# Kernel tuning notes

Measured on AMD Instinct MI355X. Metric: run time of the kernel, lower is better.

## Reference

```python
import jax, jax.numpy as jnp
import numpy as np

B, S, E = 4, 2048, 1024
H, Dh = 16, 64


def setup_inputs() -> dict:
    key = jax.random.key(0)
    ks = jax.random.split(key, 9)
    scale_in = 1.0 / np.sqrt(E)
    scale_out = 1.0 / np.sqrt(H * Dh)
    x = jax.random.normal(ks[0], (B, S, E), dtype=jnp.float32)
    # Per-head projection weights stacked over heads: [H, E, Dh]
    Wq = jax.random.uniform(ks[1], (H, E, Dh), jnp.float32, -scale_in, scale_in)
    bq = jax.random.uniform(ks[2], (H, Dh), jnp.float32, -scale_in, scale_in)
    Wk = jax.random.uniform(ks[3], (H, E, Dh), jnp.float32, -scale_in, scale_in)
    bk = jax.random.uniform(ks[4], (H, Dh), jnp.float32, -scale_in, scale_in)
    Wv = jax.random.uniform(ks[5], (H, E, Dh), jnp.float32, -scale_in, scale_in)
    bv = jax.random.uniform(ks[6], (H, Dh), jnp.float32, -scale_in, scale_in)
    # Output projection: [H*Dh, E]
    Wo = jax.random.uniform(ks[7], (H * Dh, E), jnp.float32, -scale_out, scale_out)
    bo = jax.random.uniform(ks[8], (E,), jnp.float32, -scale_out, scale_out)
    return {"x": x, "Wq": Wq, "bq": bq, "Wk": Wk, "bk": bk,
            "Wv": Wv, "bv": bv, "Wo": Wo, "bo": bo}


def reference(x, Wq, bq, Wk, bk, Wv, bv, Wo, bo):
    # Per-head linear projections, batched over heads: [B, H, S, Dh]
    q = jnp.einsum('bse,hed->bhsd', x, Wq) + bq[None, :, None, :]
    k = jnp.einsum('bse,hed->bhsd', x, Wk) + bk[None, :, None, :]
    v = jnp.einsum('bse,hed->bhsd', x, Wv) + bv[None, :, None, :]
    scale = 1.0 / jnp.sqrt(jnp.asarray(Dh, dtype=x.dtype))
    scores = jnp.einsum('bhsd,bhtd->bhst', q, k) * scale  # [B, H, S, S]
    weights = jax.nn.softmax(scores, axis=-1)
    z = jnp.einsum('bhst,bhtd->bhsd', weights, v)  # [B, H, S, Dh]
    # Concat heads in module order: [B, S, H*Dh]
    z = jnp.transpose(z, (0, 2, 1, 3)).reshape(B, S, H * Dh)
    return z @ Wo + bo
```

## Files before the change

### kernel.cpp

```cpp
#include <hip/hip_runtime.h>
#include <hip/hip_bf16.h>

#define B_  4
#define S_  2048
#define E_  1024
#define H_  16
#define DH_ 64
#define M_  (B_*S_)
#define HD_ (H_*DH_)

typedef unsigned short u16;
typedef __attribute__((ext_vector_type(8))) __bf16 bf16x8;
typedef __attribute__((ext_vector_type(4))) __bf16 bf16x4;
typedef __attribute__((ext_vector_type(4))) float  f32x4;

#if __has_builtin(__builtin_amdgcn_exp2f)
#define EXP2F __builtin_amdgcn_exp2f
#else
#define EXP2F __builtin_exp2f
#endif

#define QSCALE 0.18033688011112042f

__device__ __forceinline__ void g2l16(const void* g, void* l) {
  __builtin_amdgcn_global_load_lds(
      (const __attribute__((address_space(1))) void*)g,
      (__attribute__((address_space(3))) void*)l, 16, 0, 0);
}

__device__ __forceinline__ u16 f2bf(float f) {
  union { float f; unsigned u; } v; v.f = f;
  unsigned r = v.u + 0x7FFFu + ((v.u >> 16) & 1u);
  return (u16)(r >> 16);
}

__global__ __launch_bounds__(256) void prep_kernel(
    const float* __restrict__ x, const float* __restrict__ Wq,
    const float* __restrict__ Wk, const float* __restrict__ Wv,
    const float* __restrict__ Wo,
    u16* __restrict__ xb, u16* __restrict__ wqkvT, u16* __restrict__ woT) {
  __shared__ u16 tile[64][66];
  const int blk = blockIdx.x, tid = threadIdx.x;
  if (blk < 8192) {
    int i = blk * 256 + tid;
    float4 v = ((const float4*)x)[i];
    ushort4 o;
    o.x = f2bf(v.x); o.y = f2bf(v.y); o.z = f2bf(v.z); o.w = f2bf(v.w);
    ((ushort4*)xb)[i] = o;
  } else if (blk < 8960) {
    int b2 = blk - 8192;
    int p = b2 >> 8, h = (b2 >> 4) & 15, e0 = (b2 & 15) * 64;
    const float* src = (p == 0 ? Wq : (p == 1 ? Wk : Wv)) + h * (E_ * DH_);
#pragma unroll
    for (int r = 0; r < 16; ++r) {
      int idx = r * 256 + tid;
      int el = idx >> 6, d = idx & 63;
      tile[el][d] = f2bf(src[(e0 + el) * DH_ + d]);
    }
    __syncthreads();
    u16* dst = wqkvT + (p * HD_ + h * DH_) * E_;
#pragma unroll
    for (int r = 0; r < 16; ++r) {
      int idx = r * 256 + tid;
      int d = idx >> 6, el = idx & 63;
      dst[d * E_ + e0 + el] = tile[el][d];
    }
  } else {
    int b3 = blk - 8960;
    int c0 = (b3 >> 4) * 64, e0 = (b3 & 15) * 64;
#pragma unroll
    for (int r = 0; r < 16; ++r) {
      int idx = r * 256 + tid;
      int cl = idx >> 6, el = idx & 63;
      tile[cl][el] = f2bf(Wo[(c0 + cl) * E_ + e0 + el]);
    }
    __syncthreads();
#pragma unroll
    for (int r = 0; r < 16; ++r) {
      int idx = r * 256 + tid;
      int er = idx >> 6, cl = idx & 63;
      woT[(e0 + er) * HD_ + c0 + cl] = tile[cl][er];
    }
  }
}

__global__ __launch_bounds__(256) void transpose_v_kernel(
    const u16* __restrict__ vin, u16* __restrict__ vout) {
  __shared__ u16 t[64][72];
  const int tid = threadIdx.x;
  const int bh = blockIdx.y, st = blockIdx.x * 64;
  const u16* src = vin + ((size_t)((bh >> 4) * S_ + st)) * HD_ + (bh & 15) * 64;
#pragma unroll
  for (int rr = 0; rr < 2; ++rr) {
    int idx = rr * 256 + tid;
    int s = idx >> 3, ch = idx & 7;
    *(uint4*)&t[s][ch * 8] = *(const uint4*)(src + s * HD_ + ch * 8);
  }
  __syncthreads();
  u16* dst = vout + ((size_t)bh) * DH_ * S_ + st;
#pragma unroll
  for (int rr = 0; rr < 2; ++rr) {
    int idx = rr * 256 + tid;
    int d = idx >> 3, sc = (idx & 7) * 8;
    ushort4 o0, o1;
    o0.x = t[sc + 0][d]; o0.y = t[sc + 1][d]; o0.z = t[sc + 2][d]; o0.w = t[sc + 3][d];
    o1.x = t[sc + 4][d]; o1.y = t[sc + 5][d]; o1.z = t[sc + 6][d]; o1.w = t[sc + 7][d];
    *(ushort4*)(dst + (size_t)d * S_ + sc) = o0;
    *(ushort4*)(dst + (size_t)d * S_ + sc + 4) = o1;
  }
}

template <int MODE>
__global__ __launch_bounds__(256) void gemm_bt_kernel(
    const u16* __restrict__ A, const u16* __restrict__ Bt,
    const float* __restrict__ b0, const float* __restrict__ b1,
    const float* __restrict__ b2,
    u16* __restrict__ oQ, u16* __restrict__ oK, u16* __restrict__ oV,
    float* __restrict__ oF) {
  constexpr int K = 1024;
  __shared__ __align__(16) u16 As[128 * 64];
  __shared__ __align__(16) u16 Bs[128 * 64];
  const int tid = threadIdx.x;
  const int lane = tid & 63, wv = tid >> 6;
  const int wm = (wv >> 1) * 64, wn = (wv & 1) * 64;
  const int q4 = lane >> 4, lm = lane & 15;
  const int tileM = blockIdx.y * 128, tileN = blockIdx.x * 128;

  const u16* gA[4]; const u16* gB[4]; u16* lA[4]; u16* lB[4];
#pragma unroll
  for (int rr = 0; rr < 4; ++rr) {
    int c = rr * 256 + tid;
    int r = c >> 3, sw = ((c & 7) ^ (r & 7)) * 8;
    gA[rr] = A + (size_t)(tileM + r) * K + sw;
    gB[rr] = Bt + (size_t)(tileN + r) * K + sw;
    lA[rr] = As + c * 8;
    lB[rr] = Bs + c * 8;
  }

  f32x4 acc[4][4] = {};

  int aoff[2][4], boff[2][4];
#pragma unroll
  for (int ks = 0; ks < 2; ++ks) {
#pragma unroll
    for (int i = 0; i < 4; ++i) {
      int ra = wm + i * 16 + lm;
      aoff[ks][i] = ra * 64 + (((ks * 4 + q4) ^ (ra & 7)) * 8);
      int rb = wn + i * 16 + lm;
      boff[ks][i] = rb * 64 + (((ks * 4 + q4) ^ (rb & 7)) * 8);
    }
  }

  for (int k0 = 0; k0 < K; k0 += 64) {
#pragma unroll
    for (int rr = 0; rr < 4; ++rr) {
      g2l16(gA[rr] + k0, lA[rr]);
      g2l16(gB[rr] + k0, lB[rr]);
    }
    __syncthreads();
#pragma unroll
    for (int ks = 0; ks < 2; ++ks) {
      bf16x8 af[4], bf[4];
#pragma unroll
      for (int i = 0; i < 4; ++i) af[i] = *(const bf16x8*)(As + aoff[ks][i]);
#pragma unroll
      for (int j = 0; j < 4; ++j) bf[j] = *(const bf16x8*)(Bs + boff[ks][j]);
#pragma unroll
      for (int i = 0; i < 4; ++i)
#pragma unroll
        for (int j = 0; j < 4; ++j)
          acc[i][j] = __builtin_amdgcn_mfma_f32_16x16x32_bf16(af[i], bf[j], acc[i][j], 0, 0, 0);
    }
    __syncthreads();
  }

#pragma unroll
  for (int j = 0; j < 4; ++j) {
    int n = tileN + wn + j * 16 + lm;
    float bs;
    int proj = 0, cc = n;
    if (MODE == 1) {
      bs = b0[n];
    } else {
      proj = n >> 10; cc = n & 1023;
      const float* bp = (proj == 0 ? b0 : (proj == 1 ? b1 : b2));
      bs = bp[cc];
    }
#pragma unroll
    for (int i = 0; i < 4; ++i) {
      int m0 = tileM + wm + i * 16 + q4 * 4;
      if (MODE == 1) {
#pragma unroll
        for (int r = 0; r < 4; ++r) oF[(m0 + r) * HD_ + n] = acc[i][j][r] + bs;
      } else {
        u16* optr = (proj == 0 ? oQ : (proj == 1 ? oK : oV));
        float scl = (proj == 0 ? QSCALE : 1.0f);
        f32x4 vv;
#pragma unroll
        for (int r = 0; r < 4; ++r) vv[r] = (acc[i][j][r] + bs) * scl;
        bf16x4 ov = __builtin_convertvector(vv, bf16x4);
        ushort4 us = *(ushort4*)&ov;
        optr[(m0 + 0) * 1024 + cc] = us.x;
        optr[(m0 + 1) * 1024 + cc] = us.y;
        optr[(m0 + 2) * 1024 + cc] = us.z;
        optr[(m0 + 3) * 1024 + cc] = us.w;
      }
    }
  }
}

__global__ __launch_bounds__(256, 2) void flash_kernel(
    const u16* __restrict__ Q, const u16* __restrict__ Kb,
    const u16* __restrict__ Vt, u16* __restrict__ Z) {
  __shared__ __align__(16) u16 Ks[2][64 * 64];
  __shared__ __align__(16) u16 Vs[2][64 * 64];
  const int tid = threadIdx.x, lane = tid & 63, wv = tid >> 6;
  const int q4 = lane >> 4, lm = lane & 15;

  const int bid = blockIdx.x;
  const int bh = bid >> 3, qt = bid & 7;
  const int b = bh >> 4, h = bh & 15;

  const u16* qbase = Q + ((size_t)(b * S_ + qt * 256)) * HD_ + h * DH_;
  const u16* kbase = Kb + (size_t)b * S_ * HD_ + h * DH_;
  const u16* vbase = Vt + ((size_t)(b * H_ + h)) * DH_ * S_;
  u16* zbase = Z + ((size_t)(b * S_ + qt * 256)) * HD_ + h * DH_;

  const int c0 = tid,       r0 = c0 >> 3, s0 = ((c0 & 7) ^ (r0 & 7)) * 8;
  const int c1 = tid + 256, r1 = c1 >> 3, s1 = ((c1 & 7) ^ (r1 & 7)) * 8;
  const int kr0 = ((r0 >> 4) & 1) * 32 + ((r0 >> 2) & 3) * 8 + (r0 >> 5) * 4 + (r0 & 3);
  const int kr1 = ((r1 >> 4) & 1) * 32 + ((r1 >> 2) & 3) * 8 + (r1 >> 5) * 4 + (r1 & 3);

  bf16x8 qf[4][2];
#pragma unroll
  for (int qs = 0; qs < 4; ++qs)
#pragma unroll
    for (int dc = 0; dc < 2; ++dc)
      qf[qs][dc] = *(const bf16x8*)(qbase + (wv * 64 + qs * 16 + lm) * HD_ + dc * 32 + q4 * 8);

  const bf16x8 ones = {(__bf16)1.f, (__bf16)1.f, (__bf16)1.f, (__bf16)1.f,
                       (__bf16)1.f, (__bf16)1.f, (__bf16)1.f, (__bf16)1.f};

  int koff[4][2], voff[2][4];
#pragma unroll
  for (int kb = 0; kb < 4; ++kb)
#pragma unroll
    for (int dc = 0; dc < 2; ++dc) {
      int row = kb * 16 + lm;
      koff[kb][dc] = row * 64 + (((dc * 4 + q4) ^ (row & 7)) * 8);
    }
#pragma unroll
  for (int ck = 0; ck < 2; ++ck)
#pragma unroll
    for (int db = 0; db < 4; ++db) {
      int row = db * 16 + lm;
      voff[ck][db] = row * 64 + (((ck * 4 + q4) ^ (row & 7)) * 8);
    }

  f32x4 oacc[4][4] = {};
  f32x4 liacc[4] = {};

  {
    g2l16(kbase + kr0 * HD_ + s0, Ks[0] + c0 * 8);
    g2l16(kbase + kr1 * HD_ + s1, Ks[0] + c1 * 8);
    g2l16(vbase + r0 * S_ + s0, Vs[0] + c0 * 8);
    g2l16(vbase + r1 * S_ + s1, Vs[0] + c1 * 8);
  }

  for (int t = 0; t < 32; ++t) {
    const int pb = t & 1;
    __syncthreads();
    if (t < 31) {
      const u16* kt = kbase + (size_t)(t + 1) * 64 * HD_;
      const u16* vt = vbase + (t + 1) * 64;
      g2l16(kt + kr0 * HD_ + s0, Ks[1 - pb] + c0 * 8);
      g2l16(kt + kr1 * HD_ + s1, Ks[1 - pb] + c1 * 8);
      g2l16(vt + r0 * S_ + s0, Vs[1 - pb] + c0 * 8);
      g2l16(vt + r1 * S_ + s1, Vs[1 - pb] + c1 * 8);
    }
    const u16* Kp = Ks[pb];
    const u16* Vp = Vs[pb];

#pragma unroll
    for (int ck = 0; ck < 2; ++ck) {
      bf16x8 ka0 = *(const bf16x8*)(Kp + koff[ck][0]);
      bf16x8 ka1 = *(const bf16x8*)(Kp + koff[ck][1]);
      bf16x8 kb0 = *(const bf16x8*)(Kp + koff[ck + 2][0]);
      bf16x8 kb1 = *(const bf16x8*)(Kp + koff[ck + 2][1]);
      bf16x8 pf[4];
#pragma unroll
      for (int qs = 0; qs < 4; ++qs) {
        f32x4 sa = {}, sb = {};
        sa = __builtin_amdgcn_mfma_f32_16x16x32_bf16(ka0, qf[qs][0], sa, 0, 0, 0);
        sa = __builtin_amdgcn_mfma_f32_16x16x32_bf16(ka1, qf[qs][1], sa, 0, 0, 0);
        sb = __builtin_amdgcn_mfma_f32_16x16x32_bf16(kb0, qf[qs][0], sb, 0, 0, 0);
        sb = __builtin_amdgcn_mfma_f32_16x16x32_bf16(kb1, qf[qs][1], sb, 0, 0, 0);
        f32x4 pa, pb2;
#pragma unroll
        for (int r = 0; r < 4; ++r) { pa[r] = EXP2F(sa[r]); pb2[r] = EXP2F(sb[r]); }
        bf16x4 la = __builtin_convertvector(pa, bf16x4);
        bf16x4 lb = __builtin_convertvector(pb2, bf16x4);
        pf[qs] = __builtin_shufflevector(la, lb, 0, 1, 2, 3, 4, 5, 6, 7);
      }
#pragma unroll
      for (int qs = 0; qs < 4; ++qs)
        liacc[qs] = __builtin_amdgcn_mfma_f32_16x16x32_bf16(pf[qs], ones, liacc[qs], 0, 0, 0);
#pragma unroll
      for (int db = 0; db < 4; ++db) {
        bf16x8 vf = *(const bf16x8*)(Vp + voff[ck][db]);
#pragma unroll
        for (int qs = 0; qs < 4; ++qs)
          oacc[qs][db] = __builtin_amdgcn_mfma_f32_16x16x32_bf16(pf[qs], vf, oacc[qs][db], 0, 0, 0);
      }
    }
  }

#pragma unroll
  for (int qs = 0; qs < 4; ++qs) {
    float rin[4];
#pragma unroll
    for (int r = 0; r < 4; ++r) rin[r] = 1.f / liacc[qs][r];
#pragma unroll
    for (int db = 0; db < 4; ++db) {
      f32x4 vv;
#pragma unroll
      for (int r = 0; r < 4; ++r) vv[r] = oacc[qs][db][r] * rin[r];
      bf16x4 ov = __builtin_convertvector(vv, bf16x4);
      ushort4 us = *(ushort4*)&ov;
      int m0 = wv * 64 + qs * 16 + q4 * 4;
      zbase[(m0 + 0) * HD_ + db * 16 + lm] = us.x;
      zbase[(m0 + 1) * HD_ + db * 16 + lm] = us.y;
      zbase[(m0 + 2) * HD_ + db * 16 + lm] = us.z;
      zbase[(m0 + 3) * HD_ + db * 16 + lm] = us.w;
    }
  }
}

extern "C" void kernel_launch(void* const* d_in, const int* in_sizes, int n_in,
                              void* d_out, int out_size, void* d_ws, size_t ws_size,
                              hipStream_t stream) {
  const float* x  = (const float*)d_in[0];
  const float* Wq = (const float*)d_in[1];
  const float* bq = (const float*)d_in[2];
  const float* Wk = (const float*)d_in[3];
  const float* bk = (const float*)d_in[4];
  const float* Wv = (const float*)d_in[5];
  const float* bv = (const float*)d_in[6];
  const float* Wo = (const float*)d_in[7];
  const float* bo = (const float*)d_in[8];
  float* out = (float*)d_out;

  char* w = (char*)d_ws;
  u16*   xb    = (u16*)w;   w += (size_t)M_ * E_ * 2;
  u16*   wqkvT = (u16*)w;   w += (size_t)3 * HD_ * E_ * 2;
  u16*   woT   = (u16*)w;   w += (size_t)E_ * HD_ * 2;
  u16*   qB    = (u16*)w;   w += (size_t)M_ * HD_ * 2;
  u16*   kB    = (u16*)w;   w += (size_t)M_ * HD_ * 2;
  u16*   vT    = (u16*)w;   w += (size_t)M_ * HD_ * 2;
  u16*   zB    = (u16*)w;   w += (size_t)M_ * HD_ * 2;
  u16*   vB    = zB;

  prep_kernel<<<dim3(9216), 256, 0, stream>>>(x, Wq, Wk, Wv, Wo, xb, wqkvT, woT);
  gemm_bt_kernel<0><<<dim3(24, 64), 256, 0, stream>>>(xb, wqkvT, bq, bk, bv,
                                                      qB, kB, vB, nullptr);
  transpose_v_kernel<<<dim3(32, 64), 256, 0, stream>>>(vB, vT);
  flash_kernel<<<dim3(512), 256, 0, stream>>>(qB, kB, vT, zB);
  gemm_bt_kernel<1><<<dim3(8, 64), 256, 0, stream>>>(zB, woT, bo, nullptr, nullptr,
                                                     nullptr, nullptr, nullptr, out);
}
```

Baseline: 266.5 us.

## Split flash attention over KV halves, fuse V transpose into QKV GEMM epilogue

The QKV GEMM epilogue now stages each tile in LDS and writes Q/K with coalesced 16-byte stores, and writes V directly in transposed layout. This removes the separate V transpose kernel. Flash attention is split into two KV halves (1024 blocks, launch bounds raised to 4 waves per SIMD) that write unnormalized partial outputs and row sums. A new combine kernel adds the two halves and normalizes them. The goal is better occupancy and fewer, more coalesced stores, at the cost of an extra pass over the partial outputs. The split only works because the kernel has no running max, so unnormalized partials in bf16 can simply be summed.

```diff
diff --git a/kernel.cpp b/kernel.cpp
--- a/kernel.cpp
+++ b/kernel.cpp
@@ -32,6 +32,10 @@
   union { float f; unsigned u; } v; v.f = f;
   unsigned r = v.u + 0x7FFFu + ((v.u >> 16) & 1u);
   return (u16)(r >> 16);
+}
+
+__device__ __forceinline__ float bf2f(u16 u) {
+  union { unsigned u; float f; } v; v.u = ((unsigned)u) << 16; return v.f;
 }
 
 __global__ __launch_bounds__(256) void prep_kernel(
@@ -84,32 +88,6 @@
   }
 }
 
-__global__ __launch_bounds__(256) void transpose_v_kernel(
-    const u16* __restrict__ vin, u16* __restrict__ vout) {
-  __shared__ u16 t[64][72];
-  const int tid = threadIdx.x;
-  const int bh = blockIdx.y, st = blockIdx.x * 64;
-  const u16* src = vin + ((size_t)((bh >> 4) * S_ + st)) * HD_ + (bh & 15) * 64;
-#pragma unroll
-  for (int rr = 0; rr < 2; ++rr) {
-    int idx = rr * 256 + tid;
-    int s = idx >> 3, ch = idx & 7;
-    *(uint4*)&t[s][ch * 8] = *(const uint4*)(src + s * HD_ + ch * 8);
-  }
-  __syncthreads();
-  u16* dst = vout + ((size_t)bh) * DH_ * S_ + st;
-#pragma unroll
-  for (int rr = 0; rr < 2; ++rr) {
-    int idx = rr * 256 + tid;
-    int d = idx >> 3, sc = (idx & 7) * 8;
-    ushort4 o0, o1;
-    o0.x = t[sc + 0][d]; o0.y = t[sc + 1][d]; o0.z = t[sc + 2][d]; o0.w = t[sc + 3][d];
-    o1.x = t[sc + 4][d]; o1.y = t[sc + 5][d]; o1.z = t[sc + 6][d]; o1.w = t[sc + 7][d];
-    *(ushort4*)(dst + (size_t)d * S_ + sc) = o0;
-    *(ushort4*)(dst + (size_t)d * S_ + sc + 4) = o1;
-  }
-}
-
 template <int MODE>
 __global__ __launch_bounds__(256) void gemm_bt_kernel(
     const u16* __restrict__ A, const u16* __restrict__ Bt,
@@ -118,8 +96,9 @@
     u16* __restrict__ oQ, u16* __restrict__ oK, u16* __restrict__ oV,
     float* __restrict__ oF) {
   constexpr int K = 1024;
-  __shared__ __align__(16) u16 As[128 * 64];
-  __shared__ __align__(16) u16 Bs[128 * 64];
+  __shared__ __align__(16) u16 smem[2 * 128 * 64];
+  u16* As = smem;
+  u16* Bs = smem + 128 * 64;
   const int tid = threadIdx.x;
   const int lane = tid & 63, wv = tid >> 6;
   const int wm = (wv >> 1) * 64, wn = (wv & 1) * 64;
@@ -174,57 +153,90 @@
     __syncthreads();
   }
 
-#pragma unroll
-  for (int j = 0; j < 4; ++j) {
-    int n = tileN + wn + j * 16 + lm;
-    float bs;
-    int proj = 0, cc = n;
-    if (MODE == 1) {
-      bs = b0[n];
-    } else {
-      proj = n >> 10; cc = n & 1023;
-      const float* bp = (proj == 0 ? b0 : (proj == 1 ? b1 : b2));
-      bs = bp[cc];
-    }
-#pragma unroll
-    for (int i = 0; i < 4; ++i) {
-      int m0 = tileM + wm + i * 16 + q4 * 4;
-      if (MODE == 1) {
+  if (MODE == 1) {
+#pragma unroll
+    for (int j = 0; j < 4; ++j) {
+      int n = tileN + wn + j * 16 + lm;
+      float bs = b0[n];
+#pragma unroll
+      for (int i = 0; i < 4; ++i) {
+        int m0 = tileM + wm + i * 16 + q4 * 4;
 #pragma unroll
         for (int r = 0; r < 4; ++r) oF[(m0 + r) * HD_ + n] = acc[i][j][r] + bs;
-      } else {
-        u16* optr = (proj == 0 ? oQ : (proj == 1 ? oK : oV));
-        float scl = (proj == 0 ? QSCALE : 1.0f);
+      }
+    }
+  } else {
+    u16* TT = smem;
+    const int ccb = tileN & 1023;
+    const int proj = tileN >> 10;
+    const float scl = (proj == 0 ? QSCALE : 1.0f);
+    const float* bp = (proj == 0 ? b0 : (proj == 1 ? b1 : b2));
+#pragma unroll
+    for (int j = 0; j < 4; ++j) {
+      int ncl = wn + j * 16 + lm;
+      float bs = bp[ccb + ncl];
+#pragma unroll
+      for (int i = 0; i < 4; ++i) {
+        int m0 = wm + i * 16 + q4 * 4;
         f32x4 vv;
 #pragma unroll
         for (int r = 0; r < 4; ++r) vv[r] = (acc[i][j][r] + bs) * scl;
         bf16x4 ov = __builtin_convertvector(vv, bf16x4);
-        ushort4 us = *(ushort4*)&ov;
-        optr[(m0 + 0) * 1024 + cc] = us.x;
-        optr[(m0 + 1) * 1024 + cc] = us.y;
-        optr[(m0 + 2) * 1024 + cc] = us.z;
-        optr[(m0 + 3) * 1024 + cc] = us.w;
-      }
-    }
-  }
-}
-
-__global__ __launch_bounds__(256, 2) void flash_kernel(
+        if (proj < 2) {
+          ushort4 us = *(ushort4*)&ov;
+          TT[(m0 + 0) * 128 + (ncl ^ (8 * ((m0 + 0) & 15)))] = us.x;
+          TT[(m0 + 1) * 128 + (ncl ^ (8 * ((m0 + 1) & 15)))] = us.y;
+          TT[(m0 + 2) * 128 + (ncl ^ (8 * ((m0 + 2) & 15)))] = us.z;
+          TT[(m0 + 3) * 128 + (ncl ^ (8 * ((m0 + 3) & 15)))] = us.w;
+        } else {
+          *(bf16x4*)(TT + ncl * 128 + (m0 ^ (8 * (ncl & 15)))) = ov;
+        }
+      }
+    }
+    __syncthreads();
+    if (proj < 2) {
+      u16* optr = (proj == 0 ? oQ : oK);
+#pragma unroll
+      for (int rr = 0; rr < 8; ++rr) {
+        int seg = rr * 256 + tid;
+        int ml = seg >> 4, sc = (seg & 15) * 8;
+        uint4 val = *(const uint4*)(TT + ml * 128 + (sc ^ (8 * (ml & 15))));
+        *(uint4*)(optr + (size_t)(tileM + ml) * 1024 + ccb + sc) = val;
+      }
+    } else {
+      const int bb = tileM >> 11, s0 = tileM & 2047;
+#pragma unroll
+      for (int rr = 0; rr < 8; ++rr) {
+        int seg = rr * 256 + tid;
+        int ccl = seg >> 4, sc = (seg & 15) * 8;
+        int cc = ccb + ccl;
+        int hh = cc >> 6, dd = cc & 63;
+        uint4 val = *(const uint4*)(TT + ccl * 128 + (sc ^ (8 * (ccl & 15))));
+        *(uint4*)(oV + ((size_t)(bb * 16 + hh) * 64 + dd) * 2048 + s0 + sc) = val;
+      }
+    }
+  }
+}
+
+__global__ __launch_bounds__(256, 4) void flash_kernel(
     const u16* __restrict__ Q, const u16* __restrict__ Kb,
-    const u16* __restrict__ Vt, u16* __restrict__ Z) {
+    const u16* __restrict__ Vt,
+    u16* __restrict__ O0, u16* __restrict__ O1, float* __restrict__ liW) {
   __shared__ __align__(16) u16 Ks[2][64 * 64];
   __shared__ __align__(16) u16 Vs[2][64 * 64];
   const int tid = threadIdx.x, lane = tid & 63, wv = tid >> 6;
   const int q4 = lane >> 4, lm = lane & 15;
 
   const int bid = blockIdx.x;
-  const int bh = bid >> 3, qt = bid & 7;
+  const int bh = bid >> 4, qt = (bid >> 1) & 7, sp = bid & 1;
   const int b = bh >> 4, h = bh & 15;
+  const int tbase = sp * 16;
 
   const u16* qbase = Q + ((size_t)(b * S_ + qt * 256)) * HD_ + h * DH_;
   const u16* kbase = Kb + (size_t)b * S_ * HD_ + h * DH_;
   const u16* vbase = Vt + ((size_t)(b * H_ + h)) * DH_ * S_;
-  u16* zbase = Z + ((size_t)(b * S_ + qt * 256)) * HD_ + h * DH_;
+  u16* obase = (sp ? O1 : O0) + ((size_t)(b * S_ + qt * 256)) * HD_ + h * DH_;
+  float* libase = liW + sp * (64 * 2048) + bh * 2048 + qt * 256;
 
   const int c0 = tid,       r0 = c0 >> 3, s0 = ((c0 & 7) ^ (r0 & 7)) * 8;
   const int c1 = tid + 256, r1 = c1 >> 3, s1 = ((c1 & 7) ^ (r1 & 7)) * 8;
@@ -261,18 +273,20 @@
   f32x4 liacc[4] = {};
 
   {
-    g2l16(kbase + kr0 * HD_ + s0, Ks[0] + c0 * 8);
-    g2l16(kbase + kr1 * HD_ + s1, Ks[0] + c1 * 8);
-    g2l16(vbase + r0 * S_ + s0, Vs[0] + c0 * 8);
-    g2l16(vbase + r1 * S_ + s1, Vs[0] + c1 * 8);
-  }
-
-  for (int t = 0; t < 32; ++t) {
+    const u16* kt = kbase + (size_t)tbase * 64 * HD_;
+    const u16* vt = vbase + tbase * 64;
+    g2l16(kt + kr0 * HD_ + s0, Ks[0] + c0 * 8);
+    g2l16(kt + kr1 * HD_ + s1, Ks[0] + c1 * 8);
+    g2l16(vt + r0 * S_ + s0, Vs[0] + c0 * 8);
+    g2l16(vt + r1 * S_ + s1, Vs[0] + c1 * 8);
+  }
+
+  for (int t = 0; t < 16; ++t) {
     const int pb = t & 1;
     __syncthreads();
-    if (t < 31) {
-      const u16* kt = kbase + (size_t)(t + 1) * 64 * HD_;
-      const u16* vt = vbase + (t + 1) * 64;
+    if (t < 15) {
+      const u16* kt = kbase + (size_t)(tbase + t + 1) * 64 * HD_;
+      const u16* vt = vbase + (tbase + t + 1) * 64;
       g2l16(kt + kr0 * HD_ + s0, Ks[1 - pb] + c0 * 8);
       g2l16(kt + kr1 * HD_ + s1, Ks[1 - pb] + c1 * 8);
       g2l16(vt + r0 * S_ + s0, Vs[1 - pb] + c0 * 8);
@@ -317,23 +331,53 @@
 
 #pragma unroll
   for (int qs = 0; qs < 4; ++qs) {
-    float rin[4];
-#pragma unroll
-    for (int r = 0; r < 4; ++r) rin[r] = 1.f / liacc[qs][r];
 #pragma unroll
     for (int db = 0; db < 4; ++db) {
-      f32x4 vv;
-#pragma unroll
-      for (int r = 0; r < 4; ++r) vv[r] = oacc[qs][db][r] * rin[r];
-      bf16x4 ov = __builtin_convertvector(vv, bf16x4);
+      bf16x4 ov = __builtin_convertvector(oacc[qs][db], bf16x4);
       ushort4 us = *(ushort4*)&ov;
       int m0 = wv * 64 + qs * 16 + q4 * 4;
-      zbase[(m0 + 0) * HD_ + db * 16 + lm] = us.x;
-      zbase[(m0 + 1) * HD_ + db * 16 + lm] = us.y;
-      zbase[(m0 + 2) * HD_ + db * 16 + lm] = us.z;
-      zbase[(m0 + 3) * HD_ + db * 16 + lm] = us.w;
-    }
-  }
+      obase[(m0 + 0) * HD_ + db * 16 + lm] = us.x;
+      obase[(m0 + 1) * HD_ + db * 16 + lm] = us.y;
+      obase[(m0 + 2) * HD_ + db * 16 + lm] = us.z;
+      obase[(m0 + 3) * HD_ + db * 16 + lm] = us.w;
+    }
+  }
+  if (lm == 0) {
+#pragma unroll
+    for (int qs = 0; qs < 4; ++qs)
+#pragma unroll
+      for (int r = 0; r < 4; ++r)
+        libase[wv * 64 + qs * 16 + q4 * 4 + r] = liacc[qs][r];
+  }
+}
+
+__global__ __launch_bounds__(256) void combine_kernel(
+    const u16* __restrict__ o1, u16* o2z, const float* __restrict__ li) {
+  const int tid = threadIdx.x;
+  const int row = blockIdx.x * 2 + (tid >> 7);
+  const int c0 = (tid & 127) * 8;
+  const int bh = (row >> 11) * 16 + (c0 >> 6);
+  const int s = row & 2047;
+  const float l = li[bh * 2048 + s] + li[64 * 2048 + bh * 2048 + s];
+  const float rin = 1.f / l;
+  const size_t off = (size_t)row * 1024 + c0;
+  ushort4 a0 = *(const ushort4*)(o1 + off);
+  ushort4 a1 = *(const ushort4*)(o1 + off + 4);
+  ushort4 b0 = *(const ushort4*)(o2z + off);
+  ushort4 b1 = *(const ushort4*)(o2z + off + 4);
+  f32x4 v0, v1;
+  v0[0] = (bf2f(a0.x) + bf2f(b0.x)) * rin;
+  v0[1] = (bf2f(a0.y) + bf2f(b0.y)) * rin;
+  v0[2] = (bf2f(a0.z) + bf2f(b0.z)) * rin;
+  v0[3] = (bf2f(a0.w) + bf2f(b0.w)) * rin;
+  v1[0] = (bf2f(a1.x) + bf2f(b1.x)) * rin;
+  v1[1] = (bf2f(a1.y) + bf2f(b1.y)) * rin;
+  v1[2] = (bf2f(a1.z) + bf2f(b1.z)) * rin;
+  v1[3] = (bf2f(a1.w) + bf2f(b1.w)) * rin;
+  bf16x4 z0 = __builtin_convertvector(v0, bf16x4);
+  bf16x4 z1 = __builtin_convertvector(v1, bf16x4);
+  *(bf16x4*)(o2z + off) = z0;
+  *(bf16x4*)(o2z + off + 4) = z1;
 }
 
 extern "C" void kernel_launch(void* const* d_in, const int* in_sizes, int n_in,
@@ -358,13 +402,14 @@
   u16*   kB    = (u16*)w;   w += (size_t)M_ * HD_ * 2;
   u16*   vT    = (u16*)w;   w += (size_t)M_ * HD_ * 2;
   u16*   zB    = (u16*)w;   w += (size_t)M_ * HD_ * 2;
-  u16*   vB    = zB;
+  u16*   o1    = xb;
+  float* liW   = (float*)wqkvT;
 
   prep_kernel<<<dim3(9216), 256, 0, stream>>>(x, Wq, Wk, Wv, Wo, xb, wqkvT, woT);
   gemm_bt_kernel<0><<<dim3(24, 64), 256, 0, stream>>>(xb, wqkvT, bq, bk, bv,
-                                                      qB, kB, vB, nullptr);
-  transpose_v_kernel<<<dim3(32, 64), 256, 0, stream>>>(vB, vT);
-  flash_kernel<<<dim3(512), 256, 0, stream>>>(qB, kB, vT, zB);
+                                                      qB, kB, vT, nullptr);
+  flash_kernel<<<dim3(1024), 256, 0, stream>>>(qB, kB, vT, o1, zB, liW);
+  combine_kernel<<<dim3(4096), 256, 0, stream>>>(o1, zB, liW);
   gemm_bt_kernel<1><<<dim3(8, 64), 256, 0, stream>>>(zB, woT, bo, nullptr, nullptr,
                                                      nullptr, nullptr, nullptr, out);
 }
```

Result: slower. 600.4 us (+125.3%).

## Fuse V transpose into QKV GEMM epilogue via swizzled LDS staging

Applied to the files above, without the earlier changes.

The QKV projection epilogue now stages each output tile in shared memory with an XOR swizzle. Q and K are then written as coalesced 16-byte row stores, and V is written directly in transposed [B,H,Dh,S] layout. This removes the separate transpose_v kernel launch and its extra global round trip of V. It also replaces the scattered 2-byte stores of the old epilogue. In exchange the epilogue gains an extra barrier and LDS traffic.

```diff
diff --git a/kernel.cpp b/kernel.cpp
--- a/kernel.cpp
+++ b/kernel.cpp
@@ -84,32 +84,6 @@
   }
 }
 
-__global__ __launch_bounds__(256) void transpose_v_kernel(
-    const u16* __restrict__ vin, u16* __restrict__ vout) {
-  __shared__ u16 t[64][72];
-  const int tid = threadIdx.x;
-  const int bh = blockIdx.y, st = blockIdx.x * 64;
-  const u16* src = vin + ((size_t)((bh >> 4) * S_ + st)) * HD_ + (bh & 15) * 64;
-#pragma unroll
-  for (int rr = 0; rr < 2; ++rr) {
-    int idx = rr * 256 + tid;
-    int s = idx >> 3, ch = idx & 7;
-    *(uint4*)&t[s][ch * 8] = *(const uint4*)(src + s * HD_ + ch * 8);
-  }
-  __syncthreads();
-  u16* dst = vout + ((size_t)bh) * DH_ * S_ + st;
-#pragma unroll
-  for (int rr = 0; rr < 2; ++rr) {
-    int idx = rr * 256 + tid;
-    int d = idx >> 3, sc = (idx & 7) * 8;
-    ushort4 o0, o1;
-    o0.x = t[sc + 0][d]; o0.y = t[sc + 1][d]; o0.z = t[sc + 2][d]; o0.w = t[sc + 3][d];
-    o1.x = t[sc + 4][d]; o1.y = t[sc + 5][d]; o1.z = t[sc + 6][d]; o1.w = t[sc + 7][d];
-    *(ushort4*)(dst + (size_t)d * S_ + sc) = o0;
-    *(ushort4*)(dst + (size_t)d * S_ + sc + 4) = o1;
-  }
-}
-
 template <int MODE>
 __global__ __launch_bounds__(256) void gemm_bt_kernel(
     const u16* __restrict__ A, const u16* __restrict__ Bt,
@@ -118,8 +92,9 @@
     u16* __restrict__ oQ, u16* __restrict__ oK, u16* __restrict__ oV,
     float* __restrict__ oF) {
   constexpr int K = 1024;
-  __shared__ __align__(16) u16 As[128 * 64];
-  __shared__ __align__(16) u16 Bs[128 * 64];
+  __shared__ __align__(16) u16 smem[2 * 128 * 64];
+  u16* As = smem;
+  u16* Bs = smem + 128 * 64;
   const int tid = threadIdx.x;
   const int lane = tid & 63, wv = tid >> 6;
   const int wm = (wv >> 1) * 64, wn = (wv & 1) * 64;
@@ -174,36 +149,66 @@
     __syncthreads();
   }
 
-#pragma unroll
-  for (int j = 0; j < 4; ++j) {
-    int n = tileN + wn + j * 16 + lm;
-    float bs;
-    int proj = 0, cc = n;
-    if (MODE == 1) {
-      bs = b0[n];
-    } else {
-      proj = n >> 10; cc = n & 1023;
-      const float* bp = (proj == 0 ? b0 : (proj == 1 ? b1 : b2));
-      bs = bp[cc];
-    }
-#pragma unroll
-    for (int i = 0; i < 4; ++i) {
-      int m0 = tileM + wm + i * 16 + q4 * 4;
-      if (MODE == 1) {
+  if (MODE == 1) {
+#pragma unroll
+    for (int j = 0; j < 4; ++j) {
+      int n = tileN + wn + j * 16 + lm;
+      float bs = b0[n];
+#pragma unroll
+      for (int i = 0; i < 4; ++i) {
+        int m0 = tileM + wm + i * 16 + q4 * 4;
 #pragma unroll
         for (int r = 0; r < 4; ++r) oF[(m0 + r) * HD_ + n] = acc[i][j][r] + bs;
-      } else {
-        u16* optr = (proj == 0 ? oQ : (proj == 1 ? oK : oV));
-        float scl = (proj == 0 ? QSCALE : 1.0f);
+      }
+    }
+  } else {
+    u16* TT = smem;
+    const int ccb = tileN & 1023;
+    const int proj = tileN >> 10;
+    const float scl = (proj == 0 ? QSCALE : 1.0f);
+    const float* bp = (proj == 0 ? b0 : (proj == 1 ? b1 : b2));
+#pragma unroll
+    for (int j = 0; j < 4; ++j) {
+      int ncl = wn + j * 16 + lm;
+      float bs = bp[ccb + ncl];
+#pragma unroll
+      for (int i = 0; i < 4; ++i) {
+        int m0 = wm + i * 16 + q4 * 4;
         f32x4 vv;
 #pragma unroll
         for (int r = 0; r < 4; ++r) vv[r] = (acc[i][j][r] + bs) * scl;
         bf16x4 ov = __builtin_convertvector(vv, bf16x4);
-        ushort4 us = *(ushort4*)&ov;
-        optr[(m0 + 0) * 1024 + cc] = us.x;
-        optr[(m0 + 1) * 1024 + cc] = us.y;
-        optr[(m0 + 2) * 1024 + cc] = us.z;
-        optr[(m0 + 3) * 1024 + cc] = us.w;
+        if (proj < 2) {
+          ushort4 us = *(ushort4*)&ov;
+          TT[(m0 + 0) * 128 + (ncl ^ (8 * ((m0 + 0) & 15)))] = us.x;
+          TT[(m0 + 1) * 128 + (ncl ^ (8 * ((m0 + 1) & 15)))] = us.y;
+          TT[(m0 + 2) * 128 + (ncl ^ (8 * ((m0 + 2) & 15)))] = us.z;
+          TT[(m0 + 3) * 128 + (ncl ^ (8 * ((m0 + 3) & 15)))] = us.w;
+        } else {
+          *(bf16x4*)(TT + ncl * 128 + (m0 ^ (8 * (ncl & 15)))) = ov;
+        }
+      }
+    }
+    __syncthreads();
+    if (proj < 2) {
+      u16* optr = (proj == 0 ? oQ : oK);
+#pragma unroll
+      for (int rr = 0; rr < 8; ++rr) {
+        int seg = rr * 256 + tid;
+        int ml = seg >> 4, sc = (seg & 15) * 8;
+        uint4 val = *(const uint4*)(TT + ml * 128 + (sc ^ (8 * (ml & 15))));
+        *(uint4*)(optr + (size_t)(tileM + ml) * 1024 + ccb + sc) = val;
+      }
+    } else {
+      const int bb = tileM >> 11, s0 = tileM & 2047;
+#pragma unroll
+      for (int rr = 0; rr < 8; ++rr) {
+        int seg = rr * 256 + tid;
+        int ccl = seg >> 4, sc = (seg & 15) * 8;
+        int cc = ccb + ccl;
+        int hh = cc >> 6, dd = cc & 63;
+        uint4 val = *(const uint4*)(TT + ccl * 128 + (sc ^ (8 * (ccl & 15))));
+        *(uint4*)(oV + ((size_t)(bb * 16 + hh) * 64 + dd) * 2048 + s0 + sc) = val;
       }
     }
   }
@@ -358,12 +363,10 @@
   u16*   kB    = (u16*)w;   w += (size_t)M_ * HD_ * 2;
   u16*   vT    = (u16*)w;   w += (size_t)M_ * HD_ * 2;
   u16*   zB    = (u16*)w;   w += (size_t)M_ * HD_ * 2;
-  u16*   vB    = zB;
 
   prep_kernel<<<dim3(9216), 256, 0, stream>>>(x, Wq, Wk, Wv, Wo, xb, wqkvT, woT);
   gemm_bt_kernel<0><<<dim3(24, 64), 256, 0, stream>>>(xb, wqkvT, bq, bk, bv,
-                                                      qB, kB, vB, nullptr);
-  transpose_v_kernel<<<dim3(32, 64), 256, 0, stream>>>(vB, vT);
+                                                      qB, kB, vT, nullptr);
   flash_kernel<<<dim3(512), 256, 0, stream>>>(qB, kB, vT, zB);
   gemm_bt_kernel<1><<<dim3(8, 64), 256, 0, stream>>>(zB, woT, bo, nullptr, nullptr,
                                                      nullptr, nullptr, nullptr, out);
```

Result: faster. 259.8 us (-2.5%).
